# Kernel tuning notes

Measured on AMD Instinct MI355X. Metric: run time of the kernel, lower is better.

Reference implementation:

```python
import jax, jax.numpy as jnp
import numpy as np


def _kernels(r):
    """Build the 8 normalized directional box kernels, shape [8,1,k,k]."""
    k = 2 * r + 1
    ones = np.ones((k, k), np.float32)
    L = ones.copy(); L[:, r + 1:] = 0
    R = ones.copy(); R[:, :r] = 0
    U = ones.copy(); U[r + 1:, :] = 0
    D = ones.copy(); D[:r, :] = 0
    NW = U.copy(); NW[:, r + 1:] = 0
    NE = U.copy(); NE[:, :r] = 0
    SW = D.copy(); SW[:, r + 1:] = 0
    SE = D.copy(); SE[:, :r] = 0
    half = np.float32((r + 1) * k)
    quad = np.float32((r + 1) ** 2)
    ker = np.stack([L / half, R / half, U / half, D / half,
                    NW / quad, NE / quad, SW / quad, SE / quad])
    return jnp.asarray(ker[:, None, :, :])  # [8,1,k,k]


def setup_inputs() -> dict:
    key = jax.random.key(0)
    im = jax.random.uniform(key, (4, 3, 1024, 1024), dtype=jnp.float32)
    return {"im": im, "radius": 7, "iteration": 3}


def reference(im, radius, iteration):
    W = _kernels(radius)                      # [8,1,k,k] constants
    b, c, h, w = im.shape
    # channels are filtered independently -> fold channel into batch
    x = im.reshape(b * c, 1, h, w)
    pad = [(radius, radius), (radius, radius)]

    def step(x, _):
        # 8 directional box means minus center pixel: [bc,8,h,w]
        d = jax.lax.conv_general_dilated(
            x, W, window_strides=(1, 1), padding=pad,
            dimension_numbers=("NCHW", "OIHW", "NCHW")) - x
        idx = jnp.argmin(jnp.abs(d), axis=1, keepdims=True)  # [bc,1,h,w]
        dm = jnp.take_along_axis(d, idx, axis=1)
        return x + dm, None

    x, _ = jax.lax.scan(step, x, None, length=iteration)
    return x.reshape(b, c, h, w)
```

## Files before the change

### kernel.cpp

```cpp
#include <hip/hip_runtime.h>

#define HH 1024
#define WW 1024
#define NIMG 12

__device__ __forceinline__ float fwd8(float a) {
  a += __shfl_down(a, 1, 64);
  a += __shfl_down(a, 2, 64);
  a += __shfl_down(a, 4, 64);
  return a;
}
__device__ __forceinline__ float bwd8(float a) {
  a += __shfl_up(a, 1, 64);
  a += __shfl_up(a, 2, 64);
  a += __shfl_up(a, 4, 64);
  return a;
}

struct RowLd { float v0, v1, wc; };

__device__ __forceinline__ RowLd row_load(const float* __restrict__ s, int ry, int col) {
  RowLd t;
  if ((unsigned)ry < (unsigned)HH) {
    const float* r = s + (size_t)ry * WW;
    t.v0 = (col >= 7) ? r[col - 7] : 0.0f;
    t.v1 = (col + 7 < WW) ? r[col + 7] : 0.0f;
    t.wc = r[col];
  } else { t.v0 = 0.0f; t.v1 = 0.0f; t.wc = 0.0f; }
  return t;
}

__device__ __forceinline__ void row_combine(const RowLd& t, int lane,
                                            float& lh, float& rh, float& w) {
  float lf = fwd8(t.v0);
  float lb = bwd8(t.wc);
  bool lo = (lane <= 56);
  lh = lo ? lf : lb;
  float rsh = __shfl_down(lh, 7, 64);
  float rb  = bwd8(t.v1);
  rh = lo ? rsh : rb;
  w  = t.wc;
}

__device__ __forceinline__ float winner(float a, float b) {
  return (fabsf(b) < fabsf(a)) ? b : a;
}

__device__ __forceinline__ float out_px(float ua, float ub, float uc,
                                        float da, float db, float dc,
                                        float lh0, float rh0, float w0) {
  const float ih = 1.0f / 120.0f, iq = 1.0f / 64.0f;
  const float nw0 = -w0;
  const float Ls = ua + da - lh0;
  const float Rs = ub + db - rh0;
  const float Us = ua + ub - uc;
  const float Ds = da + db - dc;
  float d0 = fmaf(Ls, ih, nw0);
  float d1 = fmaf(Rs, ih, nw0);
  float d2 = fmaf(Us, ih, nw0);
  float d3 = fmaf(Ds, ih, nw0);
  float d4 = fmaf(ua, iq, nw0);
  float d5 = fmaf(ub, iq, nw0);
  float d6 = fmaf(da, iq, nw0);
  float d7 = fmaf(db, iq, nw0);
  float w01 = winner(d0, d1), w23 = winner(d2, d3);
  float w45 = winner(d4, d5), w67 = winner(d6, d7);
  float bd = winner(winner(w01, w23), winner(w45, w67));
  return w0 + bd;
}

__global__ __launch_bounds__(256, 4) void swf_step(const float* __restrict__ src,
                                                   float* __restrict__ dst) {
  const int lane = threadIdx.x & 63;
  const int wid  = threadIdx.x >> 6;
  const int col  = blockIdx.x * 64 + lane;
  const int y0   = (blockIdx.y * 4 + wid) * 32;
  const float* s = src + (size_t)blockIdx.z * HH * WW;
  float* d       = dst + (size_t)blockIdx.z * HH * WW;

  float rlh[16], rrh[16], rw[16];

  #pragma unroll
  for (int j = 0; j < 15; ++j) {
    const int slot = (j + 8) & 15;
    RowLd t = row_load(s, y0 - 8 + j, col);
    row_combine(t, lane, rlh[slot], rrh[slot], rw[slot]);
  }

  float ua = 0.f, ub = 0.f, uc = 0.f, da = 0.f, db = 0.f, dc = 0.f;
  #pragma unroll
  for (int j = 0; j < 8; ++j) {
    const int sl = (8 + j) & 15;
    ua += rlh[sl]; ub += rrh[sl]; uc += rw[sl];
  }
  #pragma unroll
  for (int j = 0; j < 8; ++j) {
    const int sl = (15 + j) & 15;
    da += rlh[sl]; db += rrh[sl]; dc += rw[sl];
  }

  RowLd pipe[8];
  #pragma unroll
  for (int k = 0; k < 4; ++k) pipe[k] = row_load(s, y0 + 7 + k, col);

  #pragma unroll 1
  for (int yb = 0; yb < 32; yb += 16) {
    #pragma unroll
    for (int i = 0; i < 16; i += 2) {
      const int y = y0 + yb + i;
      pipe[(i + 4) & 7] = row_load(s, y + 11, col);
      pipe[(i + 5) & 7] = row_load(s, y + 12, col);

      const int ls0 = (i + 7) & 15;
      const int ls1 = (i + 8) & 15;
      row_combine(pipe[i & 7], lane, rlh[ls0], rrh[ls0], rw[ls0]);
      float lh1, rh1, w1;
      row_combine(pipe[(i + 1) & 7], lane, lh1, rh1, w1);

      ua += rlh[i];   ua -= rlh[ls1];
      ub += rrh[i];   ub -= rrh[ls1];
      uc += rw [i];   uc -= rw [ls1];
      da += rlh[ls0]; da -= rlh[(i + 15) & 15];
      db += rrh[ls0]; db -= rrh[(i + 15) & 15];
      dc += rw [ls0]; dc -= rw [(i + 15) & 15];
      const float o0 = out_px(ua, ub, uc, da, db, dc, rlh[i], rrh[i], rw[i]);

      rlh[ls1] = lh1; rrh[ls1] = rh1; rw[ls1] = w1;

      const int i1 = i + 1;
      ua += rlh[i1];  ua -= rlh[(i1 + 8) & 15];
      ub += rrh[i1];  ub -= rrh[(i1 + 8) & 15];
      uc += rw [i1];  uc -= rw [(i1 + 8) & 15];
      da += rlh[ls1]; da -= rlh[i];
      db += rrh[ls1]; db -= rrh[i];
      dc += rw [ls1]; dc -= rw [i];
      const float o1 = out_px(ua, ub, uc, da, db, dc, rlh[i1], rrh[i1], rw[i1]);

      d[(size_t)y * WW + col]       = o0;
      d[(size_t)(y + 1) * WW + col] = o1;
    }
  }
}

extern "C" void kernel_launch(void* const* d_in, const int* in_sizes, int n_in,
                              void* d_out, int out_size, void* d_ws, size_t ws_size,
                              hipStream_t stream) {
  const float* in = (const float*)d_in[0];
  float* out = (float*)d_out;
  float* ws  = (float*)d_ws;

  dim3 grid(WW / 64, 8, NIMG);
  dim3 block(256);

  swf_step<<<grid, block, 0, stream>>>(in, out);
  swf_step<<<grid, block, 0, stream>>>(out, ws);
  swf_step<<<grid, block, 0, stream>>>(ws, out);
}
```

Measured before the change: 144.7 us.

## Use overlapping column strips with halo lanes instead of cross-wave edge loads

Each wavefront now loads a single value per row from a 64-wide column window that includes a 7-pixel halo on each side, and writes only the 50 interior columns. Grid x shrinks to 21 strips. This removes the three loads per row (left, right, centre) and the extra backward shuffle reductions, replacing them with one load, one forward 8-sum and one shuffle-up. In exchange, about 22% of lanes do redundant compute and never store, and the last strip is partly out of range. The prefetch depth is also increased from 4 to 6 rows.

Result: faster. 123.0 us (-15.0%).

```diff
diff --git a/kernel.cpp b/kernel.cpp
--- a/kernel.cpp
+++ b/kernel.cpp
@@ -3,6 +3,8 @@
 #define HH 1024
 #define WW 1024
 #define NIMG 12
+#define OUTC 50
+#define NSTRIP 21
 
 __device__ __forceinline__ float fwd8(float a) {
   a += __shfl_down(a, 1, 64);
@@ -10,36 +12,11 @@
   a += __shfl_down(a, 4, 64);
   return a;
 }
-__device__ __forceinline__ float bwd8(float a) {
-  a += __shfl_up(a, 1, 64);
-  a += __shfl_up(a, 2, 64);
-  a += __shfl_up(a, 4, 64);
-  return a;
-}
 
-struct RowLd { float v0, v1, wc; };
-
-__device__ __forceinline__ RowLd row_load(const float* __restrict__ s, int ry, int col) {
-  RowLd t;
-  if ((unsigned)ry < (unsigned)HH) {
-    const float* r = s + (size_t)ry * WW;
-    t.v0 = (col >= 7) ? r[col - 7] : 0.0f;
-    t.v1 = (col + 7 < WW) ? r[col + 7] : 0.0f;
-    t.wc = r[col];
-  } else { t.v0 = 0.0f; t.v1 = 0.0f; t.wc = 0.0f; }
-  return t;
-}
-
-__device__ __forceinline__ void row_combine(const RowLd& t, int lane,
-                                            float& lh, float& rh, float& w) {
-  float lf = fwd8(t.v0);
-  float lb = bwd8(t.wc);
-  bool lo = (lane <= 56);
-  lh = lo ? lf : lb;
-  float rsh = __shfl_down(lh, 7, 64);
-  float rb  = bwd8(t.v1);
-  rh = lo ? rsh : rb;
-  w  = t.wc;
+__device__ __forceinline__ float load_px(const float* __restrict__ s, int ry, int cl) {
+  if ((unsigned)ry < (unsigned)HH && (unsigned)cl < (unsigned)WW)
+    return s[(size_t)ry * WW + cl];
+  return 0.0f;
 }
 
 __device__ __forceinline__ float winner(float a, float b) {
@@ -73,18 +50,24 @@
                                                    float* __restrict__ dst) {
   const int lane = threadIdx.x & 63;
   const int wid  = threadIdx.x >> 6;
-  const int col  = blockIdx.x * 64 + lane;
+  const int cl   = blockIdx.x * OUTC - 7 + lane;
   const int y0   = (blockIdx.y * 4 + wid) * 32;
   const float* s = src + (size_t)blockIdx.z * HH * WW;
   float* d       = dst + (size_t)blockIdx.z * HH * WW;
+
+  const int  colOut  = cl;
+  const bool writeOK = (lane >= 7) && (lane <= 56) && (colOut < WW);
 
   float rlh[16], rrh[16], rw[16];
 
   #pragma unroll
   for (int j = 0; j < 15; ++j) {
     const int slot = (j + 8) & 15;
-    RowLd t = row_load(s, y0 - 8 + j, col);
-    row_combine(t, lane, rlh[slot], rrh[slot], rw[slot]);
+    float wc = load_px(s, y0 - 8 + j, cl);
+    float f  = fwd8(wc);
+    rlh[slot] = __shfl_up(f, 7, 64);
+    rrh[slot] = f;
+    rw [slot] = wc;
   }
 
   float ua = 0.f, ub = 0.f, uc = 0.f, da = 0.f, db = 0.f, dc = 0.f;
@@ -99,23 +82,29 @@
     da += rlh[sl]; db += rrh[sl]; dc += rw[sl];
   }
 
-  RowLd pipe[8];
+  float pipe[8];
   #pragma unroll
-  for (int k = 0; k < 4; ++k) pipe[k] = row_load(s, y0 + 7 + k, col);
+  for (int k = 0; k < 6; ++k) pipe[k] = load_px(s, y0 + 7 + k, cl);
 
   #pragma unroll 1
   for (int yb = 0; yb < 32; yb += 16) {
     #pragma unroll
     for (int i = 0; i < 16; i += 2) {
       const int y = y0 + yb + i;
-      pipe[(i + 4) & 7] = row_load(s, y + 11, col);
-      pipe[(i + 5) & 7] = row_load(s, y + 12, col);
+      pipe[(i + 6) & 7] = load_px(s, y + 13, cl);
+      pipe[(i + 7) & 7] = load_px(s, y + 14, cl);
 
       const int ls0 = (i + 7) & 15;
       const int ls1 = (i + 8) & 15;
-      row_combine(pipe[i & 7], lane, rlh[ls0], rrh[ls0], rw[ls0]);
-      float lh1, rh1, w1;
-      row_combine(pipe[(i + 1) & 7], lane, lh1, rh1, w1);
+
+      const float t0 = pipe[i & 7];
+      const float t1 = pipe[(i + 1) & 7];
+      float f0 = fwd8(t0);
+      float f1 = fwd8(t1);
+      float l0 = __shfl_up(f0, 7, 64);
+      float l1 = __shfl_up(f1, 7, 64);
+
+      rlh[ls0] = l0; rrh[ls0] = f0; rw[ls0] = t0;
 
       ua += rlh[i];   ua -= rlh[ls1];
       ub += rrh[i];   ub -= rrh[ls1];
@@ -125,7 +114,7 @@
       dc += rw [ls0]; dc -= rw [(i + 15) & 15];
       const float o0 = out_px(ua, ub, uc, da, db, dc, rlh[i], rrh[i], rw[i]);
 
-      rlh[ls1] = lh1; rrh[ls1] = rh1; rw[ls1] = w1;
+      rlh[ls1] = l1; rrh[ls1] = f1; rw[ls1] = t1;
 
       const int i1 = i + 1;
       ua += rlh[i1];  ua -= rlh[(i1 + 8) & 15];
@@ -136,8 +125,10 @@
       dc += rw [ls1]; dc -= rw [i];
       const float o1 = out_px(ua, ub, uc, da, db, dc, rlh[i1], rrh[i1], rw[i1]);
 
-      d[(size_t)y * WW + col]       = o0;
-      d[(size_t)(y + 1) * WW + col] = o1;
+      if (writeOK) {
+        d[(size_t)y * WW + colOut]       = o0;
+        d[(size_t)(y + 1) * WW + colOut] = o1;
+      }
     }
   }
 }
@@ -149,7 +140,7 @@
   float* out = (float*)d_out;
   float* ws  = (float*)d_ws;
 
-  dim3 grid(WW / 64, 8, NIMG);
+  dim3 grid(NSTRIP, 8, NIMG);
   dim3 block(256);
 
   swf_step<<<grid, block, 0, stream>>>(in, out);
```
